# Optimization experiments

Hardware: AMD Instinct MI355X
Metric: run time of the kernel (lower is better)

The kernel has to match this reference:

```python
import jax, jax.numpy as jnp
import numpy as np

IN_SIZE = 64
RES = 1024
B = 16
T = 2048
ALPHA = 0.5
SPECTRAL_RADIUS = 0.9


def setup_inputs() -> dict:
    key = jax.random.key(0)
    ks = jax.random.split(key, 8)
    # W_hh scaled so spectral radius ~ SPECTRAL_RADIUS (circular law: |eig|max ~ sqrt(R)*std)
    scale_hh = SPECTRAL_RADIUS / np.sqrt(RES)
    return {
        "x": jax.random.normal(ks[0], (B, T, IN_SIZE), dtype=jnp.float32),
        "W_in0": jax.random.normal(ks[1], (IN_SIZE, RES), dtype=jnp.float32) * 0.5,
        "W_hh0": jax.random.normal(ks[2], (RES, RES), dtype=jnp.float32) * scale_hh,
        "b0": jax.random.normal(ks[3], (1, RES), dtype=jnp.float32) * 0.5,
        "W_in1": jax.random.normal(ks[4], (RES, RES), dtype=jnp.float32) * 0.1,
        "W_hh1": jax.random.normal(ks[5], (RES, RES), dtype=jnp.float32) * scale_hh,
        "b1": jax.random.normal(ks[6], (1, RES), dtype=jnp.float32) * 0.5,
        "readout": jax.random.normal(ks[7], (2 * RES, IN_SIZE), dtype=jnp.float32) * 0.02,
    }


def _reservoir_layer(xs, W_in, W_hh, b, alpha):
    # xs: [T, B, F] time-major; sequential leaky-integrator scan over T
    h0 = jnp.zeros((xs.shape[1], W_hh.shape[0]), dtype=xs.dtype)

    def step(h, x_i):
        h = (1.0 - alpha) * h + alpha * jnp.tanh(x_i @ W_in + h @ W_hh + b)
        return h, h

    _, states = jax.lax.scan(step, h0, xs)
    return states  # [T, B, R]


def reference(x, W_in0, W_hh0, b0, W_in1, W_hh1, b1, readout):
    xt = jnp.transpose(x, (1, 0, 2))  # [T, B, in]
    s0 = _reservoir_layer(xt, W_in0, W_hh0, b0, ALPHA)  # [T, B, R]
    s1 = _reservoir_layer(s0, W_in1, W_hh1, b1, ALPHA)  # [T, B, R]
    h = jnp.concatenate([s0, s1], axis=-1)  # [T, B, 2R]
    out = h @ readout  # [T, B, in]
    return jnp.transpose(out, (1, 0, 2))  # [B, T, in]
```

## Files before the change

kernel.cpp:

```cpp
#include <hip/hip_runtime.h>
#include <math.h>

#define ESN_B 16
#define ESN_T 2048
#define ESN_R 1024
#define ESN_IN 64
#define NBR (ESN_B * ESN_R)

#define OFF_WT_HH0 0
#define OFF_WT_IN1 (1024 * 1024)
#define OFF_WT_HH1 (2 * 1024 * 1024)
#define OFF_WT_IN0 (3 * 1024 * 1024)
#define OFF_RT     (OFF_WT_IN0 + 1024 * 64)
#define OFF_S0G    (OFF_RT + 64 * 2048)
#define OFF_S1G    (OFF_S0G + 2 * NBR)
#define OFF_FLAGS  (OFF_S1G + 2 * NBR)

__global__ void __launch_bounds__(256) transpose_k(const float* __restrict__ src,
                                                   float* __restrict__ dst,
                                                   int rows, int cols) {
  __shared__ float tile[32][33];
  int bx = blockIdx.x * 32, by = blockIdx.y * 32;
  int tx = threadIdx.x, ty = threadIdx.y;
  #pragma unroll
  for (int i = ty; i < 32; i += 8) {
    int r = by + i, c = bx + tx;
    if (r < rows && c < cols) tile[i][tx] = src[(size_t)r * cols + c];
  }
  __syncthreads();
  #pragma unroll
  for (int i = ty; i < 32; i += 8) {
    int c = bx + i, r = by + tx;
    if (c < cols && r < rows) dst[(size_t)c * rows + r] = tile[tx][i];
  }
}

__device__ __forceinline__ float fast_tanh(float v) {
  float a = fabsf(v);
  float e = __expf(-2.0f * a);
  float t = __fdividef(1.0f - e, 1.0f + e);
  return copysignf(t, v);
}

__device__ __forceinline__ float dot4(float4 a, float4 b, float acc) {
  acc = fmaf(a.x, b.x, acc);
  acc = fmaf(a.y, b.y, acc);
  acc = fmaf(a.z, b.z, acc);
  acc = fmaf(a.w, b.w, acc);
  return acc;
}

__device__ __forceinline__ float wave_red64(float v) {
  #pragma unroll
  for (int off = 32; off > 0; off >>= 1) v += __shfl_xor(v, off, 64);
  return v;
}

__device__ __forceinline__ float reduce4(float a0, float a1, float a2, float a3,
                                         bool lb0, bool lb1) {
  float uA = lb0 ? a0 : a1, kA = lb0 ? a1 : a0;
  float A = kA + __shfl_xor(uA, 1, 64);
  float uB = lb0 ? a2 : a3, kB = lb0 ? a3 : a2;
  float B = kB + __shfl_xor(uB, 1, 64);
  float uC = lb1 ? A : B, kC = lb1 ? B : A;
  float C = kC + __shfl_xor(uC, 2, 64);
  C += __shfl_xor(C, 4, 64);
  C += __shfl_xor(C, 8, 64);
  C += __shfl_xor(C, 16, 64);
  C += __shfl_xor(C, 32, 64);
  return C;
}

__device__ __forceinline__ void llc_store_f32(float* p, float v) {
  asm volatile("global_store_dword %0, %1, off sc1" :: "v"(p), "v"(v) : "memory");
}
__device__ __forceinline__ void llc_store_u32(unsigned* p, unsigned v) {
  asm volatile("global_store_dword %0, %1, off sc1" :: "v"(p), "v"(v) : "memory");
}
__device__ __forceinline__ uint4 llc_load_u32x4(const unsigned* p) {
  uint4 f;
  asm volatile("global_load_dwordx4 %0, %1, off sc1\n\ts_waitcnt vmcnt(0)"
               : "=v"(f) : "v"(p) : "memory");
  return f;
}
__device__ __forceinline__ void vmcnt0() {
  asm volatile("s_waitcnt vmcnt(0)" ::: "memory");
}

__global__ void __launch_bounds__(256, 1) esn_scan_kernel(
    const float* __restrict__ x,
    const float* __restrict__ b0,
    const float* __restrict__ b1,
    float* __restrict__ wsf,
    float* __restrict__ out) {
  __shared__ float s0l[2][4][1024];
  __shared__ float s1l[4][1024];
  extern __shared__ float dyn_pad[];
  if (blockIdx.x == 0x7fffffffu) dyn_pad[0] = 1.0f;

  const float* wtHH0 = wsf + OFF_WT_HH0;
  const float* wtIN1 = wsf + OFF_WT_IN1;
  const float* wtHH1 = wsf + OFF_WT_HH1;
  const float* wtIN0 = wsf + OFF_WT_IN0;
  const float* rt    = wsf + OFF_RT;
  float* s0g = wsf + OFF_S0G;
  float* s1g = wsf + OFF_S1G;
  unsigned* flags = (unsigned*)(wsf + OFF_FLAGS);

  const int tid = threadIdx.x;
  const int l = tid & 63;
  const int w = tid >> 6;
  const int bid = blockIdx.x;
  const int g = bid >> 6;
  const int bg = bid & 63;
  const int batch0 = g * 4;
  const int c0 = (bg * 4 + w) * 4;
  const int wg = bg * 4 + w;
  const int rbl = wg >> 6;
  const int rb = batch0 + rbl;
  const int roc = wg & 63;
  unsigned* gflags = flags + g * 256;
  const bool lb0 = (l & 1) != 0;
  const bool lb1 = (l & 2) != 0;

  float4 wA0_0, wA0_1, wA0_2, wA0_3, wA1_0, wA1_1, wA1_2, wA1_3;
  float4 wA2_0, wA2_1, wA2_2, wA2_3, wA3_0, wA3_1, wA3_2, wA3_3;
  float4 wB0_0, wB0_1, wB0_2, wB0_3, wB1_0, wB1_1, wB1_2, wB1_3;
  float4 wB2_0, wB2_1, wB2_2, wB2_3, wB3_0, wB3_1, wB3_2, wB3_3;
  float4 wC0_0, wC0_1, wC0_2, wC0_3, wC1_0, wC1_1, wC1_2, wC1_3;
  float4 wC2_0, wC2_1, wC2_2, wC2_3, wC3_0, wC3_1, wC3_2, wC3_3;
  float4 rd0, rd1, rd2, rd3, rd4, rd5, rd6, rd7;
  float wI0, wI1, wI2, wI3;

#define LOADW(cc) { \
    const float* pA = wtHH0 + (size_t)(c0 + cc) * ESN_R + l * 4; \
    const float* pB = wtIN1 + (size_t)(c0 + cc) * ESN_R + l * 4; \
    const float* pC = wtHH1 + (size_t)(c0 + cc) * ESN_R + l * 4; \
    wA##cc##_0 = *(const float4*)(pA);       wA##cc##_1 = *(const float4*)(pA + 256); \
    wA##cc##_2 = *(const float4*)(pA + 512); wA##cc##_3 = *(const float4*)(pA + 768); \
    wB##cc##_0 = *(const float4*)(pB);       wB##cc##_1 = *(const float4*)(pB + 256); \
    wB##cc##_2 = *(const float4*)(pB + 512); wB##cc##_3 = *(const float4*)(pB + 768); \
    wC##cc##_0 = *(const float4*)(pC);       wC##cc##_1 = *(const float4*)(pC + 256); \
    wC##cc##_2 = *(const float4*)(pC + 512); wC##cc##_3 = *(const float4*)(pC + 768); \
  }
  LOADW(0) LOADW(1) LOADW(2) LOADW(3)
#undef LOADW

  {
    const float* pr = rt + (size_t)roc * 2048 + l * 4;
    rd0 = *(const float4*)(pr);        rd1 = *(const float4*)(pr + 256);
    rd2 = *(const float4*)(pr + 512);  rd3 = *(const float4*)(pr + 768);
    rd4 = *(const float4*)(pr + 1024); rd5 = *(const float4*)(pr + 1280);
    rd6 = *(const float4*)(pr + 1536); rd7 = *(const float4*)(pr + 1792);
  }
  wI0 = wtIN0[(size_t)(c0 + 0) * ESN_IN + l];
  wI1 = wtIN0[(size_t)(c0 + 1) * ESN_IN + l];
  wI2 = wtIN0[(size_t)(c0 + 2) * ESN_IN + l];
  wI3 = wtIN0[(size_t)(c0 + 3) * ESN_IN + l];
  const float b0sel = b0[c0 + (l & 3)];
  const float b1sel = b1[c0 + (l & 3)];

  for (int r = 0; r < ESN_T + 2; ++r) {
    const int slot = r & 1, oslot = slot ^ 1;
    const bool doL0 = (r < ESN_T);
    const bool doL1 = (r >= 1 && r <= ESN_T);

    float xv0 = 0.f, xv1 = 0.f, xv2 = 0.f, xv3 = 0.f;
    if (doL0) {
      xv0 = x[((size_t)(batch0 + 0) * ESN_T + r) * ESN_IN + l];
      xv1 = x[((size_t)(batch0 + 1) * ESN_T + r) * ESN_IN + l];
      xv2 = x[((size_t)(batch0 + 2) * ESN_T + r) * ESN_IN + l];
      xv3 = x[((size_t)(batch0 + 3) * ESN_T + r) * ESN_IN + l];
    }

    if (r > 0) {
      if (w == 0) {
        for (;;) {
          uint4 f = llc_load_u32x4(&gflags[l * 4]);
          bool ok = f.x >= (unsigned)r && f.y >= (unsigned)r &&
                    f.z >= (unsigned)r && f.w >= (unsigned)r;
          if (__all(ok)) break;
        }
      }
      __syncthreads();
    }

    {
      const float* gs0 = s0g + oslot * NBR + batch0 * ESN_R + tid * 4;
      const float* gs1 = s1g + oslot * NBR + batch0 * ESN_R + tid * 4;
      float4 t0, t1, t2, t3, u0, u1, u2, u3;
      asm volatile(
          "global_load_dwordx4 %0, %8, off sc1\n\t"
          "global_load_dwordx4 %1, %9, off sc1\n\t"
          "global_load_dwordx4 %2, %10, off sc1\n\t"
          "global_load_dwordx4 %3, %11, off sc1\n\t"
          "global_load_dwordx4 %4, %12, off sc1\n\t"
          "global_load_dwordx4 %5, %13, off sc1\n\t"
          "global_load_dwordx4 %6, %14, off sc1\n\t"
          "global_load_dwordx4 %7, %15, off sc1\n\t"
          "s_waitcnt vmcnt(0)"
          : "=&v"(t0), "=&v"(t1), "=&v"(t2), "=&v"(t3),
            "=&v"(u0), "=&v"(u1), "=&v"(u2), "=&v"(u3)
          : "v"(gs0), "v"(gs0 + 1024), "v"(gs0 + 2048), "v"(gs0 + 3072),
            "v"(gs1), "v"(gs1 + 1024), "v"(gs1 + 2048), "v"(gs1 + 3072)
          : "memory");
      float* d0 = &s0l[slot][0][0] + tid * 4;
      float* d1 = &s1l[0][0] + tid * 4;
      *(float4*)(d0)        = t0;
      *(float4*)(d0 + 1024) = t1;
      *(float4*)(d0 + 2048) = t2;
      *(float4*)(d0 + 3072) = t3;
      *(float4*)(d1)        = u0;
      *(float4*)(d1 + 1024) = u1;
      *(float4*)(d1 + 2048) = u2;
      *(float4*)(d1 + 3072) = u3;
    }
    __syncthreads();

    for (int bb = 0; bb < 4; ++bb) {
      const float* hp = &s0l[slot][bb][l * 4];
      float4 h0x = *(const float4*)(hp);
      float4 h1x = *(const float4*)(hp + 256);
      float4 h2x = *(const float4*)(hp + 512);
      float4 h3x = *(const float4*)(hp + 768);
      float xb = (bb == 0) ? xv0 : (bb == 1) ? xv1 : (bb == 2) ? xv2 : xv3;

      if (doL0) {
        float a0 = xb * wI0, a1 = xb * wI1, a2 = xb * wI2, a3 = xb * wI3;
#define DOT_A(cc, acc) \
        acc = dot4(wA##cc##_0, h0x, acc); acc = dot4(wA##cc##_1, h1x, acc); \
        acc = dot4(wA##cc##_2, h2x, acc); acc = dot4(wA##cc##_3, h3x, acc);
        DOT_A(0, a0) DOT_A(1, a1) DOT_A(2, a2) DOT_A(3, a3)
#undef DOT_A
        float C = reduce4(a0, a1, a2, a3, lb0, lb1);
        if (l < 4) {
          float prev = s0l[slot][bb][c0 + l];
          float nv = 0.5f * prev + 0.5f * fast_tanh(C + b0sel);
          llc_store_f32(&s0g[slot * NBR + (batch0 + bb) * ESN_R + c0 + l], nv);
        }
      }
      if (doL1) {
        const float* gp = &s1l[bb][l * 4];
        float4 g0x = *(const float4*)(gp);
        float4 g1x = *(const float4*)(gp + 256);
        float4 g2x = *(const float4*)(gp + 512);
        float4 g3x = *(const float4*)(gp + 768);
        float a0 = 0.f, a1 = 0.f, a2 = 0.f, a3 = 0.f;
#define DOT_BC(cc, acc) \
        acc = dot4(wB##cc##_0, h0x, acc); acc = dot4(wB##cc##_1, h1x, acc); \
        acc = dot4(wB##cc##_2, h2x, acc); acc = dot4(wB##cc##_3, h3x, acc); \
        acc = dot4(wC##cc##_0, g0x, acc); acc = dot4(wC##cc##_1, g1x, acc); \
        acc = dot4(wC##cc##_2, g2x, acc); acc = dot4(wC##cc##_3, g3x, acc);
        DOT_BC(0, a0) DOT_BC(1, a1) DOT_BC(2, a2) DOT_BC(3, a3)
#undef DOT_BC
        float C = reduce4(a0, a1, a2, a3, lb0, lb1);
        if (l < 4) {
          float prev = s1l[bb][c0 + l];
          float nv = 0.5f * prev + 0.5f * fast_tanh(C + b1sel);
          llc_store_f32(&s1g[slot * NBR + (batch0 + bb) * ESN_R + c0 + l], nv);
        }
      }
    }

    vmcnt0();
    if (l == 0) llc_store_u32(&gflags[bg * 4 + w], (unsigned)(r + 1));

    if (r >= 2) {
      const float* sp = &s0l[oslot][rbl][l * 4];
      const float* tp = &s1l[rbl][l * 4];
      float a = 0.f;
      a = dot4(rd0, *(const float4*)(sp), a);
      a = dot4(rd1, *(const float4*)(sp + 256), a);
      a = dot4(rd2, *(const float4*)(sp + 512), a);
      a = dot4(rd3, *(const float4*)(sp + 768), a);
      a = dot4(rd4, *(const float4*)(tp), a);
      a = dot4(rd5, *(const float4*)(tp + 256), a);
      a = dot4(rd6, *(const float4*)(tp + 512), a);
      a = dot4(rd7, *(const float4*)(tp + 768), a);
      a = wave_red64(a);
      if (l == 0) out[((size_t)rb * ESN_T + (r - 2)) * ESN_IN + roc] = a;
    }
  }
}

extern "C" void kernel_launch(void* const* d_in, const int* in_sizes, int n_in,
                              void* d_out, int out_size, void* d_ws, size_t ws_size,
                              hipStream_t stream) {
  (void)in_sizes; (void)n_in; (void)out_size; (void)ws_size;
  const float* x     = (const float*)d_in[0];
  const float* w_in0 = (const float*)d_in[1];
  const float* w_hh0 = (const float*)d_in[2];
  const float* b0    = (const float*)d_in[3];
  const float* w_in1 = (const float*)d_in[4];
  const float* w_hh1 = (const float*)d_in[5];
  const float* b1    = (const float*)d_in[6];
  const float* rdo   = (const float*)d_in[7];
  float* out = (float*)d_out;
  float* wsf = (float*)d_ws;

  dim3 tb(32, 8);
  transpose_k<<<dim3(32, 32), tb, 0, stream>>>(w_hh0, wsf + OFF_WT_HH0, 1024, 1024);
  transpose_k<<<dim3(32, 32), tb, 0, stream>>>(w_in1, wsf + OFF_WT_IN1, 1024, 1024);
  transpose_k<<<dim3(32, 32), tb, 0, stream>>>(w_hh1, wsf + OFF_WT_HH1, 1024, 1024);
  transpose_k<<<dim3(32, 2),  tb, 0, stream>>>(w_in0, wsf + OFF_WT_IN0, 64, 1024);
  transpose_k<<<dim3(2, 64),  tb, 0, stream>>>(rdo,   wsf + OFF_RT, 2048, 64);

  hipMemsetAsync(wsf + OFF_S0G + NBR, 0, NBR * sizeof(float), stream);
  hipMemsetAsync(wsf + OFF_S1G, 0, NBR * sizeof(float), stream);
  hipMemsetAsync(wsf + OFF_FLAGS, 0, 4 * 256 * sizeof(unsigned), stream);

  esn_scan_kernel<<<dim3(256), dim3(256), 40960, stream>>>(x, b0, b1, wsf, out);
}
```

Measured before the change: 13.88 ms.

## Double waves per block so each wave computes two output columns

```diff
diff --git a/kernel.cpp b/kernel.cpp
--- a/kernel.cpp
+++ b/kernel.cpp
@@ -56,19 +56,15 @@
   return v;
 }
 
-__device__ __forceinline__ float reduce4(float a0, float a1, float a2, float a3,
-                                         bool lb0, bool lb1) {
-  float uA = lb0 ? a0 : a1, kA = lb0 ? a1 : a0;
-  float A = kA + __shfl_xor(uA, 1, 64);
-  float uB = lb0 ? a2 : a3, kB = lb0 ? a3 : a2;
-  float B = kB + __shfl_xor(uB, 1, 64);
-  float uC = lb1 ? A : B, kC = lb1 ? B : A;
-  float C = kC + __shfl_xor(uC, 2, 64);
-  C += __shfl_xor(C, 4, 64);
-  C += __shfl_xor(C, 8, 64);
-  C += __shfl_xor(C, 16, 64);
-  C += __shfl_xor(C, 32, 64);
-  return C;
+__device__ __forceinline__ float reduce2(float a0, float a1, bool lb0) {
+  float u = lb0 ? a0 : a1, k = lb0 ? a1 : a0;
+  float A = k + __shfl_xor(u, 1, 64);
+  A += __shfl_xor(A, 2, 64);
+  A += __shfl_xor(A, 4, 64);
+  A += __shfl_xor(A, 8, 64);
+  A += __shfl_xor(A, 16, 64);
+  A += __shfl_xor(A, 32, 64);
+  return A;
 }
 
 __device__ __forceinline__ void llc_store_f32(float* p, float v) {
@@ -77,17 +73,17 @@
 __device__ __forceinline__ void llc_store_u32(unsigned* p, unsigned v) {
   asm volatile("global_store_dword %0, %1, off sc1" :: "v"(p), "v"(v) : "memory");
 }
-__device__ __forceinline__ uint4 llc_load_u32x4(const unsigned* p) {
-  uint4 f;
-  asm volatile("global_load_dwordx4 %0, %1, off sc1\n\ts_waitcnt vmcnt(0)"
-               : "=v"(f) : "v"(p) : "memory");
-  return f;
+__device__ __forceinline__ void llc_load_flags8(const unsigned* p, uint4& a, uint4& b) {
+  asm volatile("global_load_dwordx4 %0, %2, off sc1\n\t"
+               "global_load_dwordx4 %1, %3, off sc1\n\t"
+               "s_waitcnt vmcnt(0)"
+               : "=&v"(a), "=&v"(b) : "v"(p), "v"(p + 4) : "memory");
 }
 __device__ __forceinline__ void vmcnt0() {
   asm volatile("s_waitcnt vmcnt(0)" ::: "memory");
 }
 
-__global__ void __launch_bounds__(256, 1) esn_scan_kernel(
+__global__ void __launch_bounds__(512, 2) esn_scan_kernel(
     const float* __restrict__ x,
     const float* __restrict__ b0,
     const float* __restrict__ b1,
@@ -114,23 +110,19 @@
   const int g = bid >> 6;
   const int bg = bid & 63;
   const int batch0 = g * 4;
-  const int c0 = (bg * 4 + w) * 4;
-  const int wg = bg * 4 + w;
-  const int rbl = wg >> 6;
+  const int wg = bg * 8 + w;
+  const int c0 = wg * 2;
+  const bool doRO = (wg < 256);
+  const int rbl = (wg >> 6) & 3;
   const int rb = batch0 + rbl;
   const int roc = wg & 63;
-  unsigned* gflags = flags + g * 256;
+  unsigned* gflags = flags + g * 512;
   const bool lb0 = (l & 1) != 0;
-  const bool lb1 = (l & 2) != 0;
 
   float4 wA0_0, wA0_1, wA0_2, wA0_3, wA1_0, wA1_1, wA1_2, wA1_3;
-  float4 wA2_0, wA2_1, wA2_2, wA2_3, wA3_0, wA3_1, wA3_2, wA3_3;
   float4 wB0_0, wB0_1, wB0_2, wB0_3, wB1_0, wB1_1, wB1_2, wB1_3;
-  float4 wB2_0, wB2_1, wB2_2, wB2_3, wB3_0, wB3_1, wB3_2, wB3_3;
   float4 wC0_0, wC0_1, wC0_2, wC0_3, wC1_0, wC1_1, wC1_2, wC1_3;
-  float4 wC2_0, wC2_1, wC2_2, wC2_3, wC3_0, wC3_1, wC3_2, wC3_3;
   float4 rd0, rd1, rd2, rd3, rd4, rd5, rd6, rd7;
-  float wI0, wI1, wI2, wI3;
 
 #define LOADW(cc) { \
     const float* pA = wtHH0 + (size_t)(c0 + cc) * ESN_R + l * 4; \
@@ -143,22 +135,21 @@
     wC##cc##_0 = *(const float4*)(pC);       wC##cc##_1 = *(const float4*)(pC + 256); \
     wC##cc##_2 = *(const float4*)(pC + 512); wC##cc##_3 = *(const float4*)(pC + 768); \
   }
-  LOADW(0) LOADW(1) LOADW(2) LOADW(3)
+  LOADW(0) LOADW(1)
 #undef LOADW
 
-  {
+  rd0 = rd1 = rd2 = rd3 = rd4 = rd5 = rd6 = rd7 = make_float4(0.f, 0.f, 0.f, 0.f);
+  if (doRO) {
     const float* pr = rt + (size_t)roc * 2048 + l * 4;
     rd0 = *(const float4*)(pr);        rd1 = *(const float4*)(pr + 256);
     rd2 = *(const float4*)(pr + 512);  rd3 = *(const float4*)(pr + 768);
     rd4 = *(const float4*)(pr + 1024); rd5 = *(const float4*)(pr + 1280);
     rd6 = *(const float4*)(pr + 1536); rd7 = *(const float4*)(pr + 1792);
   }
-  wI0 = wtIN0[(size_t)(c0 + 0) * ESN_IN + l];
-  wI1 = wtIN0[(size_t)(c0 + 1) * ESN_IN + l];
-  wI2 = wtIN0[(size_t)(c0 + 2) * ESN_IN + l];
-  wI3 = wtIN0[(size_t)(c0 + 3) * ESN_IN + l];
-  const float b0sel = b0[c0 + (l & 3)];
-  const float b1sel = b1[c0 + (l & 3)];
+  const float wI0 = wtIN0[(size_t)(c0 + 0) * ESN_IN + l];
+  const float wI1 = wtIN0[(size_t)(c0 + 1) * ESN_IN + l];
+  const float b0sel = b0[c0 + (l & 1)];
+  const float b1sel = b1[c0 + (l & 1)];
 
   for (int r = 0; r < ESN_T + 2; ++r) {
     const int slot = r & 1, oslot = slot ^ 1;
@@ -176,9 +167,12 @@
     if (r > 0) {
       if (w == 0) {
         for (;;) {
-          uint4 f = llc_load_u32x4(&gflags[l * 4]);
-          bool ok = f.x >= (unsigned)r && f.y >= (unsigned)r &&
-                    f.z >= (unsigned)r && f.w >= (unsigned)r;
+          uint4 fa, fb;
+          llc_load_flags8(&gflags[l * 8], fa, fb);
+          bool ok = fa.x >= (unsigned)r && fa.y >= (unsigned)r &&
+                    fa.z >= (unsigned)r && fa.w >= (unsigned)r &&
+                    fb.x >= (unsigned)r && fb.y >= (unsigned)r &&
+                    fb.z >= (unsigned)r && fb.w >= (unsigned)r;
           if (__all(ok)) break;
         }
       }
@@ -186,34 +180,24 @@
     }
 
     {
-      const float* gs0 = s0g + oslot * NBR + batch0 * ESN_R + tid * 4;
-      const float* gs1 = s1g + oslot * NBR + batch0 * ESN_R + tid * 4;
-      float4 t0, t1, t2, t3, u0, u1, u2, u3;
+      const float* p0 = s0g + oslot * NBR + batch0 * ESN_R + tid * 4;
+      const float* p1 = s1g + oslot * NBR + batch0 * ESN_R + tid * 4;
+      float4 t0, t1, u0, u1;
       asm volatile(
-          "global_load_dwordx4 %0, %8, off sc1\n\t"
-          "global_load_dwordx4 %1, %9, off sc1\n\t"
-          "global_load_dwordx4 %2, %10, off sc1\n\t"
-          "global_load_dwordx4 %3, %11, off sc1\n\t"
-          "global_load_dwordx4 %4, %12, off sc1\n\t"
-          "global_load_dwordx4 %5, %13, off sc1\n\t"
-          "global_load_dwordx4 %6, %14, off sc1\n\t"
-          "global_load_dwordx4 %7, %15, off sc1\n\t"
+          "global_load_dwordx4 %0, %4, off sc1\n\t"
+          "global_load_dwordx4 %1, %5, off sc1\n\t"
+          "global_load_dwordx4 %2, %6, off sc1\n\t"
+          "global_load_dwordx4 %3, %7, off sc1\n\t"
           "s_waitcnt vmcnt(0)"
-          : "=&v"(t0), "=&v"(t1), "=&v"(t2), "=&v"(t3),
-            "=&v"(u0), "=&v"(u1), "=&v"(u2), "=&v"(u3)
-          : "v"(gs0), "v"(gs0 + 1024), "v"(gs0 + 2048), "v"(gs0 + 3072),
-            "v"(gs1), "v"(gs1 + 1024), "v"(gs1 + 2048), "v"(gs1 + 3072)
+          : "=&v"(t0), "=&v"(t1), "=&v"(u0), "=&v"(u1)
+          : "v"(p0), "v"(p0 + 2048), "v"(p1), "v"(p1 + 2048)
           : "memory");
       float* d0 = &s0l[slot][0][0] + tid * 4;
       float* d1 = &s1l[0][0] + tid * 4;
       *(float4*)(d0)        = t0;
-      *(float4*)(d0 + 1024) = t1;
-      *(float4*)(d0 + 2048) = t2;
-      *(float4*)(d0 + 3072) = t3;
+      *(float4*)(d0 + 2048) = t1;
       *(float4*)(d1)        = u0;
-      *(float4*)(d1 + 1024) = u1;
-      *(float4*)(d1 + 2048) = u2;
-      *(float4*)(d1 + 3072) = u3;
+      *(float4*)(d1 + 2048) = u1;
     }
     __syncthreads();
 
@@ -226,14 +210,13 @@
       float xb = (bb == 0) ? xv0 : (bb == 1) ? xv1 : (bb == 2) ? xv2 : xv3;
 
       if (doL0) {
-        float a0 = xb * wI0, a1 = xb * wI1, a2 = xb * wI2, a3 = xb * wI3;
-#define DOT_A(cc, acc) \
-        acc = dot4(wA##cc##_0, h0x, acc); acc = dot4(wA##cc##_1, h1x, acc); \
-        acc = dot4(wA##cc##_2, h2x, acc); acc = dot4(wA##cc##_3, h3x, acc);
-        DOT_A(0, a0) DOT_A(1, a1) DOT_A(2, a2) DOT_A(3, a3)
-#undef DOT_A
-        float C = reduce4(a0, a1, a2, a3, lb0, lb1);
-        if (l < 4) {
+        float a0 = xb * wI0, a1 = xb * wI1;
+        a0 = dot4(wA0_0, h0x, a0); a0 = dot4(wA0_1, h1x, a0);
+        a0 = dot4(wA0_2, h2x, a0); a0 = dot4(wA0_3, h3x, a0);
+        a1 = dot4(wA1_0, h0x, a1); a1 = dot4(wA1_1, h1x, a1);
+        a1 = dot4(wA1_2, h2x, a1); a1 = dot4(wA1_3, h3x, a1);
+        float C = reduce2(a0, a1, lb0);
+        if (l < 2) {
           float prev = s0l[slot][bb][c0 + l];
           float nv = 0.5f * prev + 0.5f * fast_tanh(C + b0sel);
           llc_store_f32(&s0g[slot * NBR + (batch0 + bb) * ESN_R + c0 + l], nv);
@@ -245,16 +228,17 @@
         float4 g1x = *(const float4*)(gp + 256);
         float4 g2x = *(const float4*)(gp + 512);
         float4 g3x = *(const float4*)(gp + 768);
-        float a0 = 0.f, a1 = 0.f, a2 = 0.f, a3 = 0.f;
-#define DOT_BC(cc, acc) \
-        acc = dot4(wB##cc##_0, h0x, acc); acc = dot4(wB##cc##_1, h1x, acc); \
-        acc = dot4(wB##cc##_2, h2x, acc); acc = dot4(wB##cc##_3, h3x, acc); \
-        acc = dot4(wC##cc##_0, g0x, acc); acc = dot4(wC##cc##_1, g1x, acc); \
-        acc = dot4(wC##cc##_2, g2x, acc); acc = dot4(wC##cc##_3, g3x, acc);
-        DOT_BC(0, a0) DOT_BC(1, a1) DOT_BC(2, a2) DOT_BC(3, a3)
-#undef DOT_BC
-        float C = reduce4(a0, a1, a2, a3, lb0, lb1);
-        if (l < 4) {
+        float a0 = 0.f, a1 = 0.f;
+        a0 = dot4(wB0_0, h0x, a0); a0 = dot4(wB0_1, h1x, a0);
+        a0 = dot4(wB0_2, h2x, a0); a0 = dot4(wB0_3, h3x, a0);
+        a0 = dot4(wC0_0, g0x, a0); a0 = dot4(wC0_1, g1x, a0);
+        a0 = dot4(wC0_2, g2x, a0); a0 = dot4(wC0_3, g3x, a0);
+        a1 = dot4(wB1_0, h0x, a1); a1 = dot4(wB1_1, h1x, a1);
+        a1 = dot4(wB1_2, h2x, a1); a1 = dot4(wB1_3, h3x, a1);
+        a1 = dot4(wC1_0, g0x, a1); a1 = dot4(wC1_1, g1x, a1);
+        a1 = dot4(wC1_2, g2x, a1); a1 = dot4(wC1_3, g3x, a1);
+        float C = reduce2(a0, a1, lb0);
+        if (l < 2) {
           float prev = s1l[bb][c0 + l];
           float nv = 0.5f * prev + 0.5f * fast_tanh(C + b1sel);
           llc_store_f32(&s1g[slot * NBR + (batch0 + bb) * ESN_R + c0 + l], nv);
@@ -263,9 +247,9 @@
     }
 
     vmcnt0();
-    if (l == 0) llc_store_u32(&gflags[bg * 4 + w], (unsigned)(r + 1));
-
-    if (r >= 2) {
+    if (l == 0) llc_store_u32(&gflags[bg * 8 + w], (unsigned)(r + 1));
+
+    if (r >= 2 && doRO) {
       const float* sp = &s0l[oslot][rbl][l * 4];
       const float* tp = &s1l[rbl][l * 4];
       float a = 0.f;
@@ -307,7 +291,7 @@
 
   hipMemsetAsync(wsf + OFF_S0G + NBR, 0, NBR * sizeof(float), stream);
   hipMemsetAsync(wsf + OFF_S1G, 0, NBR * sizeof(float), stream);
-  hipMemsetAsync(wsf + OFF_FLAGS, 0, 4 * 256 * sizeof(unsigned), stream);
-
-  esn_scan_kernel<<<dim3(256), dim3(256), 40960, stream>>>(x, b0, b1, wsf, out);
-}
+  hipMemsetAsync(wsf + OFF_FLAGS, 0, 4 * 512 * sizeof(unsigned), stream);
+
+  esn_scan_kernel<<<dim3(256), dim3(512), 40960, stream>>>(x, b0, b1, wsf, out);
+}
```

Measured after the change: 16.43 ms. 1.18x slower.
